# Kernel tuning notes

Hardware: AMD Instinct MI355X
Metric: run time of the kernel (lower is better)

Reference implementation:

```python
import jax, jax.numpy as jnp
import numpy as np

N_USER = 100000
N_ITEM = 200000
N_NODES = N_USER + N_ITEM
NNZ = 4000000
EMB = 64
N_LAYERS = 3
BATCH = 4096


def setup_inputs() -> dict:
    key = jax.random.key(0)
    ks = jax.random.split(key, 12)
    inp = {
        'users': jax.random.randint(ks[0], (BATCH,), 0, N_USER, dtype=jnp.int32),
        'pos_items': jax.random.randint(ks[1], (BATCH,), 0, N_ITEM, dtype=jnp.int32),
        'neg_items': jax.random.randint(ks[2], (BATCH,), 0, N_ITEM, dtype=jnp.int32),
        'row': jax.random.randint(ks[3], (NNZ,), 0, N_NODES, dtype=jnp.int32),
        'col': jax.random.randint(ks[4], (NNZ,), 0, N_NODES, dtype=jnp.int32),
        'vals': jax.random.uniform(ks[5], (NNZ,), dtype=jnp.float32),
        'user_emb': 0.1 * jax.random.normal(ks[6], (N_USER, EMB), dtype=jnp.float32),
        'item_emb': 0.1 * jax.random.normal(ks[7], (N_ITEM, EMB), dtype=jnp.float32),
        'W_gc': 0.1 * jax.random.normal(ks[8], (N_LAYERS, EMB, EMB), dtype=jnp.float32),
        'b_gc': 0.1 * jax.random.normal(ks[9], (N_LAYERS, EMB), dtype=jnp.float32),
        'W_bi': 0.1 * jax.random.normal(ks[10], (N_LAYERS, EMB, EMB), dtype=jnp.float32),
        'b_bi': 0.1 * jax.random.normal(ks[11], (N_LAYERS, EMB), dtype=jnp.float32),
    }
    return inp


def _l2_normalize(x, eps=1e-12):
    # matches torch F.normalize(p=2, dim=1): x / max(||x||, eps)
    n = jnp.sqrt(jnp.sum(x * x, axis=1, keepdims=True))
    return x / jnp.maximum(n, eps)


def reference(users, pos_items, neg_items, row, col, vals, user_emb, item_emb, W_gc, b_gc, W_bi, b_bi):
    B = users.shape[0]
    # sparse adjacency propagation: side = A_hat @ [user_emb; item_emb]
    emb = jnp.concatenate([user_emb, item_emb], axis=0)          # [N, d]
    msgs = vals[:, None] * emb[col]                               # [nnz, d]
    side = jax.ops.segment_sum(msgs, row, num_segments=N_NODES)  # [N, d]

    u_side = side[users]                                          # [B, d]
    i_side = jnp.concatenate([side[N_USER + pos_items], side[N_USER + neg_items]], axis=0)
    small_side = jnp.concatenate([u_side, i_side], axis=0)        # [3B, d]
    ego = jnp.concatenate([user_emb[users], item_emb[pos_items], item_emb[neg_items]], axis=0)

    all_embeddings = [ego]
    for k in range(N_LAYERS):
        sum_e = small_side @ W_gc[k] + b_gc[k]
        bi = (ego * small_side) @ W_bi[k] + b_bi[k]
        ego = jax.nn.leaky_relu(sum_e + bi, negative_slope=0.2)
        all_embeddings.append(_l2_normalize(ego))

    all_e = jnp.concatenate(all_embeddings, axis=1)               # [3B, d*(L+1)]
    u_g = all_e[:B]
    i_g = all_e[B:]
    pos_g = i_g[:B]
    neg_g = i_g[B:]
    return (u_g, pos_g, neg_g)
```

## Files before the change

### kernel.cpp

```cpp
#include <hip/hip_runtime.h>

#define N_USER   100000
#define N_ITEM   200000
#define N_NODES  300000
#define NNZ      4000000
#define EMB      64
#define N_LAYERS 3
#define BATCH    4096
#define NSLOT    (3*BATCH)
#define MAXE     96
#define HCAP     256
#define BMWORDS  9376


#define CNT4   3072
#define BM4    2344

__global__ void __launch_bounds__(256) k_clear(int4* __restrict__ c4,
                                               int4* __restrict__ b4) {
    int i = blockIdx.x * blockDim.x + threadIdx.x;
    if (i < CNT4)            c4[i] = make_int4(0, 0, 0, 0);
    else if (i < CNT4 + BM4) b4[i - CNT4] = make_int4(0, 0, 0, 0);
}

__global__ void k_setup(const int* __restrict__ users,
                        const int* __restrict__ pos,
                        const int* __restrict__ neg,
                        unsigned short* __restrict__ table16,
                        unsigned int* __restrict__ bitmap) {
    int i = blockIdx.x * blockDim.x + threadIdx.x;
    if (i >= NSLOT) return;
    int node;
    if (i < BATCH)            node = users[i];
    else if (i < 2 * BATCH)   node = N_USER + pos[i - BATCH];
    else                      node = N_USER + neg[i - 2 * BATCH];
    table16[node] = (unsigned short)i;
    atomicOr(&bitmap[((unsigned)node) >> 5], 1u << (node & 31));
}

__global__ void __launch_bounds__(256) k_build(
        const int* __restrict__ row,
        const int* __restrict__ col,
        const float* __restrict__ vals,
        const unsigned int* __restrict__ bitmap,
        const unsigned short* __restrict__ table16,
        int* __restrict__ count,
        int2* __restrict__ csr2) {
    __shared__ int   ls_s[HCAP];
    __shared__ int   ls_c[HCAP];
    __shared__ float ls_v[HCAP];
    __shared__ int   cnt;
    int tid = threadIdx.x;
    if (tid == 0) cnt = 0;
    __syncthreads();

    int t = blockIdx.x * 256 + tid;
    if (t < NNZ / 4) {
        int4   r = ((const int4*)row)[t];
        int4   c = ((const int4*)col)[t];
        float4 v = ((const float4*)vals)[t];
        bool h0 = (bitmap[((unsigned)r.x) >> 5] >> (r.x & 31)) & 1;
        bool h1 = (bitmap[((unsigned)r.y) >> 5] >> (r.y & 31)) & 1;
        bool h2 = (bitmap[((unsigned)r.z) >> 5] >> (r.z & 31)) & 1;
        bool h3 = (bitmap[((unsigned)r.w) >> 5] >> (r.w & 31)) & 1;
        int rr[4] = { r.x, r.y, r.z, r.w };
        int cc[4] = { c.x, c.y, c.z, c.w };
        float vv[4] = { v.x, v.y, v.z, v.w };
        bool hh[4] = { h0, h1, h2, h3 };
        #pragma unroll
        for (int i = 0; i < 4; ++i) {
            if (hh[i]) {
                int si = (int)table16[rr[i]];
                int p = atomicAdd(&cnt, 1);
                if (p < HCAP) { ls_s[p] = si; ls_c[p] = cc[i]; ls_v[p] = vv[i]; }
                else {
                    int pp = atomicAdd(&count[si], 1);
                    if (pp < MAXE)
                        csr2[(size_t)si * MAXE + pp] = make_int2(cc[i], __float_as_int(vv[i]));
                }
            }
        }
    }
    __syncthreads();

    int n = cnt; n = (n < HCAP) ? n : HCAP;
    for (int t2 = tid; t2 < n; t2 += 256) {
        int si = ls_s[t2];
        int p = atomicAdd(&count[si], 1);
        if (p < MAXE)
            csr2[(size_t)si * MAXE + p] = make_int2(ls_c[t2], __float_as_int(ls_v[t2]));
    }
}

__global__ void __launch_bounds__(256) k_gather(
        const int* __restrict__ users,
        const int* __restrict__ pos,
        const int* __restrict__ neg,
        const float* __restrict__ user_emb,
        const float* __restrict__ item_emb,
        const unsigned short* __restrict__ table16,
        const int* __restrict__ count,
        const int2* __restrict__ csr2,
        float* __restrict__ side) {
    int tid = threadIdx.x;
    int w = tid >> 6;
    int j = tid & 63;
    int slot = blockIdx.x * 4 + w;

    int node;
    if (slot < BATCH)          node = users[slot];
    else if (slot < 2 * BATCH) node = N_USER + pos[slot - BATCH];
    else                       node = N_USER + neg[slot - 2 * BATCH];

    int wslot = (int)table16[node];
    wslot = __builtin_amdgcn_readfirstlane(wslot);
    int n = count[wslot];
    n = (n < MAXE) ? n : MAXE;
    n = __builtin_amdgcn_readfirstlane(n);
    const int2* base = csr2 + (size_t)wslot * MAXE;

    float acc = 0.f;
    for (int t0 = 0; t0 < n; t0 += 64) {
        int idx = t0 + j;
        int2 ev = make_int2(0, 0);
        if (idx < n) ev = base[idx];
        int m = n - t0; m = (m < 64) ? m : 64;
        for (int tt = 0; tt < m; tt += 16) {
            float vv[16], gg[16];
            #pragma unroll
            for (int k = 0; k < 16; ++k) {
                int  t  = tt + k;
                bool okk = t < m;
                int   cc = __shfl(ev.x, t, 64);
                float vb = __uint_as_float((unsigned)__shfl(ev.y, t, 64));
                vv[k] = okk ? vb : 0.f;
                int ci = okk ? cc : 0;
                const float* sp = (ci < N_USER) ? (user_emb + (size_t)ci * EMB)
                                                : (item_emb + (size_t)(ci - N_USER) * EMB);
                gg[k] = sp[j];
            }
            #pragma unroll
            for (int k = 0; k < 16; ++k) acc = fmaf(vv[k], gg[k], acc);
        }
    }
    side[(size_t)slot * EMB + j] = acc;
}

__global__ void __launch_bounds__(256) k_mlp(
        const int* __restrict__ users,
        const int* __restrict__ pos,
        const int* __restrict__ neg,
        const float* __restrict__ user_emb,
        const float* __restrict__ item_emb,
        const float* __restrict__ W_gc,
        const float* __restrict__ b_gc,
        const float* __restrict__ W_bi,
        const float* __restrict__ b_bi,
        const float* __restrict__ side,
        float* __restrict__ out) {
    __shared__ float wg[EMB * EMB];
    __shared__ float wb[EMB * EMB];
    int tid = threadIdx.x;
    int w = tid >> 6;
    int j = tid & 63;
    int sbase = blockIdx.x * 16 + w * 4;

    float sval[4], e[4];
    #pragma unroll
    for (int s = 0; s < 4; ++s) {
        int slot = sbase + s;
        int node;
        if (slot < BATCH)          node = users[slot];
        else if (slot < 2 * BATCH) node = N_USER + pos[slot - BATCH];
        else                       node = N_USER + neg[slot - 2 * BATCH];
        const float* erow = (node < N_USER) ? (user_emb + (size_t)node * EMB)
                                            : (item_emb + (size_t)(node - N_USER) * EMB);
        e[s]    = erow[j];
        sval[s] = side[(size_t)slot * EMB + j];
        out[(size_t)slot * 256 + j] = e[s];
    }

    for (int k = 0; k < N_LAYERS; ++k) {
        __syncthreads();
        {
            const float4* g4 = (const float4*)(W_gc + (size_t)k * EMB * EMB);
            const float4* b4 = (const float4*)(W_bi + (size_t)k * EMB * EMB);
            float4* lg = (float4*)wg;
            float4* lb = (float4*)wb;
            #pragma unroll
            for (int i2 = tid; i2 < EMB * EMB / 4; i2 += 256) { lg[i2] = g4[i2]; lb[i2] = b4[i2]; }
        }
        __syncthreads();

        float b1 = b_gc[k * EMB + j];
        float b2 = b_bi[k * EMB + j];
        float sum1[4], sum2[4], pv[4];
        #pragma unroll
        for (int s = 0; s < 4; ++s) { sum1[s] = b1; sum2[s] = b2; pv[s] = sval[s] * e[s]; }

        #pragma unroll 8
        for (int i = 0; i < EMB; ++i) {
            float wgi = wg[i * EMB + j];
            float wbi = wb[i * EMB + j];
            #pragma unroll
            for (int s = 0; s < 4; ++s) {
                float si = __uint_as_float(__builtin_amdgcn_readlane(__float_as_uint(sval[s]), i));
                float pi = __uint_as_float(__builtin_amdgcn_readlane(__float_as_uint(pv[s]),   i));
                sum1[s] = fmaf(si, wgi, sum1[s]);
                sum2[s] = fmaf(pi, wbi, sum2[s]);
            }
        }

        #pragma unroll
        for (int s = 0; s < 4; ++s) {
            float x = sum1[s] + sum2[s];
            x = (x >= 0.f) ? x : 0.2f * x;
            float sq = x * x;
            #pragma unroll
            for (int o = 32; o; o >>= 1) sq += __shfl_xor(sq, o, 64);
            float nn = fmaxf(sqrtf(sq), 1e-12f);
            out[(size_t)(sbase + s) * 256 + (k + 1) * 64 + j] = x / nn;
            e[s] = x;
        }
    }
}

extern "C" void kernel_launch(void* const* d_in, const int* in_sizes, int n_in,
                              void* d_out, int out_size, void* d_ws, size_t ws_size,
                              hipStream_t stream) {
    const int*   users    = (const int*)  d_in[0];
    const int*   pos      = (const int*)  d_in[1];
    const int*   neg      = (const int*)  d_in[2];
    const int*   row      = (const int*)  d_in[3];
    const int*   col      = (const int*)  d_in[4];
    const float* vals     = (const float*)d_in[5];
    const float* user_emb = (const float*)d_in[6];
    const float* item_emb = (const float*)d_in[7];
    const float* W_gc     = (const float*)d_in[8];
    const float* b_gc     = (const float*)d_in[9];
    const float* W_bi     = (const float*)d_in[10];
    const float* b_bi     = (const float*)d_in[11];
    float* out = (float*)d_out;

    char* ws = (char*)d_ws;
    unsigned short* table16 = (unsigned short*)ws;
    int*            count   = (int*)(ws + 600064);
    int2*           csr2    = (int2*)(ws + 649216);
    float*          side    = (float*)(ws + 10086400);
    unsigned int*   bitmap  = (unsigned int*)(ws + 13232128);

    k_clear<<<(CNT4 + BM4 + 255) / 256, 256, 0, stream>>>((int4*)count, (int4*)bitmap);
    k_setup<<<(NSLOT + 255) / 256, 256, 0, stream>>>(users, pos, neg, table16, bitmap);
    k_build<<<(NNZ / 4 + 255) / 256, 256, 0, stream>>>(row, col, vals, bitmap,
                                                       table16, count, csr2);
    k_gather<<<NSLOT / 4, 256, 0, stream>>>(users, pos, neg, user_emb, item_emb,
                                            table16, count, csr2, side);
    k_mlp<<<NSLOT / 16, 256, 0, stream>>>(users, pos, neg, user_emb, item_emb,
                                          W_gc, b_gc, W_bi, b_bi, side, out);
}
```

Baseline: 76.79 us.

## Fuse neighbor gather into MLP kernel and fold count clearing into setup

Removes the separate gather kernel: each wave of the MLP kernel now gathers the neighbor sums for its four slots itself, so the side buffer is never written to or read back from global memory. Layer-0 weights are loaded into shared memory before the gather so that load overlaps it. Clearing the per-slot counts moves into the setup kernel, and the build kernel now handles two int4 chunks per thread, halving its block count. The cost is that each wave runs four dependent gather loops in sequence across fewer blocks, which gives less parallelism for a latency-bound gather.

```diff
diff --git a/kernel.cpp b/kernel.cpp
--- a/kernel.cpp
+++ b/kernel.cpp
@@ -13,23 +13,22 @@
 #define BMWORDS  9376
 
 
-#define CNT4   3072
 #define BM4    2344
 
-__global__ void __launch_bounds__(256) k_clear(int4* __restrict__ c4,
-                                               int4* __restrict__ b4) {
+__global__ void __launch_bounds__(256) k_clear(int4* __restrict__ b4) {
     int i = blockIdx.x * blockDim.x + threadIdx.x;
-    if (i < CNT4)            c4[i] = make_int4(0, 0, 0, 0);
-    else if (i < CNT4 + BM4) b4[i - CNT4] = make_int4(0, 0, 0, 0);
+    if (i < BM4) b4[i] = make_int4(0, 0, 0, 0);
 }
 
 __global__ void k_setup(const int* __restrict__ users,
                         const int* __restrict__ pos,
                         const int* __restrict__ neg,
                         unsigned short* __restrict__ table16,
-                        unsigned int* __restrict__ bitmap) {
+                        unsigned int* __restrict__ bitmap,
+                        int* __restrict__ count) {
     int i = blockIdx.x * blockDim.x + threadIdx.x;
     if (i >= NSLOT) return;
+    count[i] = 0;
     int node;
     if (i < BATCH)            node = users[i];
     else if (i < 2 * BATCH)   node = N_USER + pos[i - BATCH];
@@ -54,29 +53,33 @@
     if (tid == 0) cnt = 0;
     __syncthreads();
 
-    int t = blockIdx.x * 256 + tid;
-    if (t < NNZ / 4) {
-        int4   r = ((const int4*)row)[t];
-        int4   c = ((const int4*)col)[t];
-        float4 v = ((const float4*)vals)[t];
-        bool h0 = (bitmap[((unsigned)r.x) >> 5] >> (r.x & 31)) & 1;
-        bool h1 = (bitmap[((unsigned)r.y) >> 5] >> (r.y & 31)) & 1;
-        bool h2 = (bitmap[((unsigned)r.z) >> 5] >> (r.z & 31)) & 1;
-        bool h3 = (bitmap[((unsigned)r.w) >> 5] >> (r.w & 31)) & 1;
-        int rr[4] = { r.x, r.y, r.z, r.w };
-        int cc[4] = { c.x, c.y, c.z, c.w };
-        float vv[4] = { v.x, v.y, v.z, v.w };
-        bool hh[4] = { h0, h1, h2, h3 };
-        #pragma unroll
-        for (int i = 0; i < 4; ++i) {
-            if (hh[i]) {
-                int si = (int)table16[rr[i]];
-                int p = atomicAdd(&cnt, 1);
-                if (p < HCAP) { ls_s[p] = si; ls_c[p] = cc[i]; ls_v[p] = vv[i]; }
-                else {
-                    int pp = atomicAdd(&count[si], 1);
-                    if (pp < MAXE)
-                        csr2[(size_t)si * MAXE + pp] = make_int2(cc[i], __float_as_int(vv[i]));
+    const int nt4 = NNZ / 4;
+    #pragma unroll
+    for (int q = 0; q < 2; ++q) {
+        int t = blockIdx.x * 512 + q * 256 + tid;
+        if (t < nt4) {
+            int4   r = ((const int4*)row)[t];
+            int4   c = ((const int4*)col)[t];
+            float4 v = ((const float4*)vals)[t];
+            bool h0 = (bitmap[((unsigned)r.x) >> 5] >> (r.x & 31)) & 1;
+            bool h1 = (bitmap[((unsigned)r.y) >> 5] >> (r.y & 31)) & 1;
+            bool h2 = (bitmap[((unsigned)r.z) >> 5] >> (r.z & 31)) & 1;
+            bool h3 = (bitmap[((unsigned)r.w) >> 5] >> (r.w & 31)) & 1;
+            int rr[4] = { r.x, r.y, r.z, r.w };
+            int cc[4] = { c.x, c.y, c.z, c.w };
+            float vv[4] = { v.x, v.y, v.z, v.w };
+            bool hh[4] = { h0, h1, h2, h3 };
+            #pragma unroll
+            for (int i = 0; i < 4; ++i) {
+                if (hh[i]) {
+                    int si = (int)table16[rr[i]];
+                    int p = atomicAdd(&cnt, 1);
+                    if (p < HCAP) { ls_s[p] = si; ls_c[p] = cc[i]; ls_v[p] = vv[i]; }
+                    else {
+                        int pp = atomicAdd(&count[si], 1);
+                        if (pp < MAXE)
+                            csr2[(size_t)si * MAXE + pp] = make_int2(cc[i], __float_as_int(vv[i]));
+                    }
                 }
             }
         }
@@ -92,61 +95,7 @@
     }
 }
 
-__global__ void __launch_bounds__(256) k_gather(
-        const int* __restrict__ users,
-        const int* __restrict__ pos,
-        const int* __restrict__ neg,
-        const float* __restrict__ user_emb,
-        const float* __restrict__ item_emb,
-        const unsigned short* __restrict__ table16,
-        const int* __restrict__ count,
-        const int2* __restrict__ csr2,
-        float* __restrict__ side) {
-    int tid = threadIdx.x;
-    int w = tid >> 6;
-    int j = tid & 63;
-    int slot = blockIdx.x * 4 + w;
-
-    int node;
-    if (slot < BATCH)          node = users[slot];
-    else if (slot < 2 * BATCH) node = N_USER + pos[slot - BATCH];
-    else                       node = N_USER + neg[slot - 2 * BATCH];
-
-    int wslot = (int)table16[node];
-    wslot = __builtin_amdgcn_readfirstlane(wslot);
-    int n = count[wslot];
-    n = (n < MAXE) ? n : MAXE;
-    n = __builtin_amdgcn_readfirstlane(n);
-    const int2* base = csr2 + (size_t)wslot * MAXE;
-
-    float acc = 0.f;
-    for (int t0 = 0; t0 < n; t0 += 64) {
-        int idx = t0 + j;
-        int2 ev = make_int2(0, 0);
-        if (idx < n) ev = base[idx];
-        int m = n - t0; m = (m < 64) ? m : 64;
-        for (int tt = 0; tt < m; tt += 16) {
-            float vv[16], gg[16];
-            #pragma unroll
-            for (int k = 0; k < 16; ++k) {
-                int  t  = tt + k;
-                bool okk = t < m;
-                int   cc = __shfl(ev.x, t, 64);
-                float vb = __uint_as_float((unsigned)__shfl(ev.y, t, 64));
-                vv[k] = okk ? vb : 0.f;
-                int ci = okk ? cc : 0;
-                const float* sp = (ci < N_USER) ? (user_emb + (size_t)ci * EMB)
-                                                : (item_emb + (size_t)(ci - N_USER) * EMB);
-                gg[k] = sp[j];
-            }
-            #pragma unroll
-            for (int k = 0; k < 16; ++k) acc = fmaf(vv[k], gg[k], acc);
-        }
-    }
-    side[(size_t)slot * EMB + j] = acc;
-}
-
-__global__ void __launch_bounds__(256) k_mlp(
+__global__ void __launch_bounds__(256) k_gmlp(
         const int* __restrict__ users,
         const int* __restrict__ pos,
         const int* __restrict__ neg,
@@ -156,7 +105,9 @@
         const float* __restrict__ b_gc,
         const float* __restrict__ W_bi,
         const float* __restrict__ b_bi,
-        const float* __restrict__ side,
+        const unsigned short* __restrict__ table16,
+        const int* __restrict__ count,
+        const int2* __restrict__ csr2,
         float* __restrict__ out) {
     __shared__ float wg[EMB * EMB];
     __shared__ float wb[EMB * EMB];
@@ -164,6 +115,15 @@
     int w = tid >> 6;
     int j = tid & 63;
     int sbase = blockIdx.x * 16 + w * 4;
+
+    {
+        const float4* g4 = (const float4*)W_gc;
+        const float4* b4 = (const float4*)W_bi;
+        float4* lg = (float4*)wg;
+        float4* lb = (float4*)wb;
+        #pragma unroll
+        for (int i2 = tid; i2 < EMB * EMB / 4; i2 += 256) { lg[i2] = g4[i2]; lb[i2] = b4[i2]; }
+    }
 
     float sval[4], e[4];
     #pragma unroll
@@ -175,22 +135,56 @@
         else                       node = N_USER + neg[slot - 2 * BATCH];
         const float* erow = (node < N_USER) ? (user_emb + (size_t)node * EMB)
                                             : (item_emb + (size_t)(node - N_USER) * EMB);
-        e[s]    = erow[j];
-        sval[s] = side[(size_t)slot * EMB + j];
+        e[s] = erow[j];
         out[(size_t)slot * 256 + j] = e[s];
+
+        int wslot = (int)table16[node];
+        wslot = __builtin_amdgcn_readfirstlane(wslot);
+        int n = count[wslot];
+        n = (n < MAXE) ? n : MAXE;
+        n = __builtin_amdgcn_readfirstlane(n);
+        const int2* base = csr2 + (size_t)wslot * MAXE;
+
+        float acc = 0.f;
+        for (int t0 = 0; t0 < n; t0 += 64) {
+            int idx = t0 + j;
+            int2 ev = make_int2(0, 0);
+            if (idx < n) ev = base[idx];
+            int m = n - t0; m = (m < 64) ? m : 64;
+            for (int tt = 0; tt < m; tt += 16) {
+                float vv[16], gg[16];
+                #pragma unroll
+                for (int k = 0; k < 16; ++k) {
+                    int  t  = tt + k;
+                    bool okk = t < m;
+                    int   cc = __shfl(ev.x, t, 64);
+                    float vb = __uint_as_float((unsigned)__shfl(ev.y, t, 64));
+                    vv[k] = okk ? vb : 0.f;
+                    int ci = okk ? cc : 0;
+                    const float* sp = (ci < N_USER) ? (user_emb + (size_t)ci * EMB)
+                                                    : (item_emb + (size_t)(ci - N_USER) * EMB);
+                    gg[k] = sp[j];
+                }
+                #pragma unroll
+                for (int k = 0; k < 16; ++k) acc = fmaf(vv[k], gg[k], acc);
+            }
+        }
+        sval[s] = acc;
     }
 
     for (int k = 0; k < N_LAYERS; ++k) {
-        __syncthreads();
-        {
+        if (k == 0) {
+            __syncthreads();
+        } else {
+            __syncthreads();
             const float4* g4 = (const float4*)(W_gc + (size_t)k * EMB * EMB);
             const float4* b4 = (const float4*)(W_bi + (size_t)k * EMB * EMB);
             float4* lg = (float4*)wg;
             float4* lb = (float4*)wb;
             #pragma unroll
             for (int i2 = tid; i2 < EMB * EMB / 4; i2 += 256) { lg[i2] = g4[i2]; lb[i2] = b4[i2]; }
-        }
-        __syncthreads();
+            __syncthreads();
+        }
 
         float b1 = b_gc[k * EMB + j];
         float b2 = b_bi[k * EMB + j];
@@ -246,15 +240,14 @@
     unsigned short* table16 = (unsigned short*)ws;
     int*            count   = (int*)(ws + 600064);
     int2*           csr2    = (int2*)(ws + 649216);
-    float*          side    = (float*)(ws + 10086400);
-    unsigned int*   bitmap  = (unsigned int*)(ws + 13232128);
-
-    k_clear<<<(CNT4 + BM4 + 255) / 256, 256, 0, stream>>>((int4*)count, (int4*)bitmap);
-    k_setup<<<(NSLOT + 255) / 256, 256, 0, stream>>>(users, pos, neg, table16, bitmap);
-    k_build<<<(NNZ / 4 + 255) / 256, 256, 0, stream>>>(row, col, vals, bitmap,
+    unsigned int*   bitmap  = (unsigned int*)(ws + 10086400);
+
+    k_clear<<<(BM4 + 255) / 256, 256, 0, stream>>>((int4*)bitmap);
+    k_setup<<<(NSLOT + 255) / 256, 256, 0, stream>>>(users, pos, neg, table16,
+                                                     bitmap, count);
+    k_build<<<(NNZ / 4 + 511) / 512, 256, 0, stream>>>(row, col, vals, bitmap,
                                                        table16, count, csr2);
-    k_gather<<<NSLOT / 4, 256, 0, stream>>>(users, pos, neg, user_emb, item_emb,
-                                            table16, count, csr2, side);
-    k_mlp<<<NSLOT / 16, 256, 0, stream>>>(users, pos, neg, user_emb, item_emb,
-                                          W_gc, b_gc, W_bi, b_bi, side, out);
-}
+    k_gmlp<<<NSLOT / 16, 256, 0, stream>>>(users, pos, neg, user_emb, item_emb,
+                                           W_gc, b_gc, W_bi, b_bi,
+                                           table16, count, csr2, out);
+}
```

Result: no change. 77.25 us (+0.6%).
